# Optimization experiments

Measured on AMD Instinct MI355X. Metric: run time of the kernel, lower is better.

## Reference

```python
import jax, jax.numpy as jnp
import numpy as np

OUT, IN = 11008, 4096
B, S = 8, 32


def setup_inputs() -> dict:
    key = jax.random.key(0)
    k_x, k_w, k_s, k_b = jax.random.split(key, 4)
    x = jax.random.normal(k_x, (B, S, IN), dtype=jnp.float32).astype(jnp.float16)
    # int8 weight storage (symmetric quant range [-128, 127])
    w_int8 = jax.random.randint(k_w, (OUT, IN), -128, 128, dtype=jnp.int32).astype(jnp.int8)
    # per-output-channel scale, small positive values typical of int8 quant
    scale = jax.random.uniform(k_s, (OUT,), dtype=jnp.float32) * 0.01 + 1e-4
    bias = (jax.random.normal(k_b, (OUT,), dtype=jnp.float32) * 0.02).astype(jnp.float16)
    return {"x": x, "w_int8": w_int8, "scale": scale, "bias": bias}


def reference(x, w_int8, scale, bias):
    # w_fp[o, i] = int8_weight[o, i] * scale[o]   (on-the-fly dequant)
    w = w_int8.astype(jnp.float32) * scale[:, None]          # [OUT, IN] fp32
    # F.linear: out = x @ w.T + bias, computed in fp32
    out = jnp.einsum('bsi,oi->bso', x.astype(jnp.float32), w) + bias.astype(jnp.float32)
    return out.astype(x.dtype)                                # cast back to x.dtype (fp16)
```

## Files before the change

kernel.cpp:

```cpp
#include <hip/hip_runtime.h>
#include <hip/hip_bf16.h>
#include <stdint.h>

typedef __attribute__((ext_vector_type(8))) __bf16 bf16x8;
typedef __attribute__((ext_vector_type(4))) float f32x4;

constexpr int K_DIM = 4096;
constexpr int N_DIM = 11008;
constexpr int M_DIM = 256;
constexpr int TN = 32;
constexpr int BK = 64;
constexpr int NT = 256;
constexpr int KT_ALL = K_DIM / BK;
constexpr int KSPLIT = 3;

__device__ __forceinline__ bf16x8 cvt8(const float4 u0, const float4 u1) {
  bf16x8 v;
  v[0] = (__bf16)u0.x; v[1] = (__bf16)u0.y; v[2] = (__bf16)u0.z; v[3] = (__bf16)u0.w;
  v[4] = (__bf16)u1.x; v[5] = (__bf16)u1.y; v[6] = (__bf16)u1.z; v[7] = (__bf16)u1.w;
  return v;
}

__global__ void cvt_x_kernel(const float* __restrict__ x, __bf16* __restrict__ ws) {
  const int t = blockIdx.x * 256 + threadIdx.x;
  const int m = t & 255;
  const int k8 = t >> 8;
  const float* src = x + (size_t)m * K_DIM + k8 * 8;
  const float4 u0 = ((const float4*)src)[0];
  const float4 u1 = ((const float4*)src)[1];
  *(bf16x8*)(ws + (size_t)t * 8) = cvt8(u0, u1);
}

template<bool USE_WS>
__global__ __launch_bounds__(NT, 3) void int8_linear_kernel(
    const float* __restrict__ x,
    const __bf16* __restrict__ xws,
    const int*   __restrict__ w,
    const float* __restrict__ scale,
    const float* __restrict__ bias,
    float*       __restrict__ out)
{
  __shared__ __bf16 Ws[2][TN * BK];

  const int tid  = threadIdx.x;
  const int lane = tid & 63;
  const int wv   = tid >> 6;
  const int quad = lane >> 4;
  const int l16  = lane & 15;
  const int n_base = blockIdx.x * TN;
  const int kc     = blockIdx.y;

  const int t0 = (kc * KT_ALL) / KSPLIT;
  const int t1 = ((kc + 1) * KT_ALL) / KSPLIT;
  const int ntile = t1 - t0;
  const int k0 = t0 * BK;

  const int wrow  = tid >> 3;
  const int wc    = tid & 7;
  const int wslot = wc ^ (wrow & 7);
  const int* wptr = w + (int64_t)(n_base + wrow) * K_DIM + k0 + wc * 8;

  const __bf16* aptr = xws + (size_t)(k0 / 8 + quad) * (M_DIM * 8) + (wv * 64 + l16) * 8;
  const float* fptr = x + (int64_t)(wv * 64 + l16) * K_DIM + k0 + quad * 8;

  f32x4 acc[4][2];
#pragma unroll
  for (int i = 0; i < 4; ++i)
#pragma unroll
    for (int j = 0; j < 2; ++j) acc[i][j] = (f32x4){0.f, 0.f, 0.f, 0.f};

  int wr[8];
  bf16x8 ar0[8], ar1[8];

  auto wload = [&](int t) {
    const int4* p = (const int4*)(wptr + t * BK);
    const int4 u0 = p[0], u1 = p[1];
    wr[0] = u0.x; wr[1] = u0.y; wr[2] = u0.z; wr[3] = u0.w;
    wr[4] = u1.x; wr[5] = u1.y; wr[6] = u1.z; wr[7] = u1.w;
  };
  auto commitW = [&](__bf16* wbuf) {
    bf16x8 v;
#pragma unroll
    for (int j = 0; j < 8; ++j) v[j] = (__bf16)(float)wr[j];
    *(bf16x8*)(wbuf + wrow * BK + wslot * 8) = v;
  };
  auto aload = [&](int t, bf16x8* ar) {
    if (USE_WS) {
#pragma unroll
      for (int ks = 0; ks < 2; ++ks)
#pragma unroll
        for (int mi = 0; mi < 4; ++mi)
          ar[ks * 4 + mi] =
              *(const bf16x8*)(aptr + (size_t)(t * 8 + ks * 4) * (M_DIM * 8) + mi * 128);
    } else {
#pragma unroll
      for (int ks = 0; ks < 2; ++ks)
#pragma unroll
        for (int mi = 0; mi < 4; ++mi) {
          const float* s = fptr + (int64_t)mi * 16 * K_DIM + t * BK + ks * 32;
          ar[ks * 4 + mi] = cvt8(((const float4*)s)[0], ((const float4*)s)[1]);
        }
    }
  };
  auto compute = [&](const bf16x8* ar, const __bf16* wbuf) {
#pragma unroll
    for (int ks = 0; ks < 2; ++ks) {
      bf16x8 b[2];
#pragma unroll
      for (int ni = 0; ni < 2; ++ni) {
        const int n = ni * 16 + l16;
        const int slot = (ks * 4 + quad) ^ (n & 7);
        b[ni] = *(const bf16x8*)(wbuf + n * BK + slot * 8);
      }
#pragma unroll
      for (int mi = 0; mi < 4; ++mi)
#pragma unroll
        for (int ni = 0; ni < 2; ++ni)
          acc[mi][ni] = __builtin_amdgcn_mfma_f32_16x16x32_bf16(
              ar[ks * 4 + mi], b[ni], acc[mi][ni], 0, 0, 0);
    }
  };

  wload(0);
  commitW(Ws[0]);
  aload(0, ar0);

  int t = 0;
  for (; t + 2 <= ntile; t += 2) {
    {
      __syncthreads();
      aload(t + 1, ar1);
      wload(t + 1);
      compute(ar0, Ws[0]);
      commitW(Ws[1]);
    }
    {
      __syncthreads();
      if (t + 2 < ntile) { aload(t + 2, ar0); wload(t + 2); }
      compute(ar1, Ws[1]);
      if (t + 2 < ntile) commitW(Ws[0]);
    }
  }
  if (t < ntile) {
    __syncthreads();
    compute(ar0, Ws[0]);
  }

#pragma unroll
  for (int ni = 0; ni < 2; ++ni) {
    const int col = n_base + ni * 16 + l16;
    const float sc = scale[col];
    const float bi = (kc == 0) ? bias[col] : 0.0f;
#pragma unroll
    for (int mi = 0; mi < 4; ++mi) {
      const int row0 = wv * 64 + mi * 16 + quad * 4;
#pragma unroll
      for (int r = 0; r < 4; ++r)
        unsafeAtomicAdd(out + (int64_t)(row0 + r) * N_DIM + col,
                        acc[mi][ni][r] * sc + bi);
    }
  }
}

extern "C" void kernel_launch(void* const* d_in, const int* in_sizes, int n_in,
                              void* d_out, int out_size, void* d_ws, size_t ws_size,
                              hipStream_t stream) {
  const float* x     = (const float*)d_in[0];
  const int*   w     = (const int*)d_in[1];
  const float* scale = (const float*)d_in[2];
  const float* bias  = (const float*)d_in[3];
  float* out = (float*)d_out;

  __bf16* xws = (__bf16*)d_ws;
  const bool use_ws = ws_size >= (size_t)M_DIM * K_DIM * sizeof(__bf16);

  hipMemsetAsync(out, 0, (size_t)M_DIM * N_DIM * sizeof(float), stream);

  dim3 grid(N_DIM / TN, KSPLIT), block(NT);
  if (use_ws) {
    cvt_x_kernel<<<M_DIM * K_DIM / (256 * 8), 256, 0, stream>>>(x, xws);
    int8_linear_kernel<true><<<grid, block, 0, stream>>>(x, xws, w, scale, bias, out);
  } else {
    int8_linear_kernel<false><<<grid, block, 0, stream>>>(x, xws, w, scale, bias, out);
  }
}
```

Measured before the change: 304.9 us.

## Stage activations in LDS with direct global-to-LDS loads and widen N tile

The N tile grows from 32 to 128 columns and the 256-row activation tile is now staged in shared memory through global_load_lds with an XOR swizzle, instead of each wave loading A fragments into registers. The activation workspace becomes plain row-major, so the conversion kernel simplifies. Split-K rises from 3 to 6 and the occupancy hint drops from 3 to 2. The aim is to reuse each A tile across more columns and cut the redundant global activation traffic. In exchange there are more accumulator registers, two barriers per k-step, and A staging that is no longer double-buffered, so load latency is less hidden.

```diff
diff --git a/kernel.cpp b/kernel.cpp
--- a/kernel.cpp
+++ b/kernel.cpp
@@ -8,11 +8,18 @@
 constexpr int K_DIM = 4096;
 constexpr int N_DIM = 11008;
 constexpr int M_DIM = 256;
-constexpr int TN = 32;
+constexpr int TM = 256;
+constexpr int TN = 128;
 constexpr int BK = 64;
 constexpr int NT = 256;
 constexpr int KT_ALL = K_DIM / BK;
-constexpr int KSPLIT = 3;
+constexpr int KSPLIT = 6;
+
+__device__ __forceinline__ void gload_lds16(const __bf16* gptr, __bf16* lptr) {
+  __builtin_amdgcn_global_load_lds(
+      (const __attribute__((address_space(1))) uint32_t*)gptr,
+      (__attribute__((address_space(3))) uint32_t*)lptr, 16, 0, 0);
+}
 
 __device__ __forceinline__ bf16x8 cvt8(const float4 u0, const float4 u1) {
   bf16x8 v;
@@ -22,17 +29,14 @@
 }
 
 __global__ void cvt_x_kernel(const float* __restrict__ x, __bf16* __restrict__ ws) {
-  const int t = blockIdx.x * 256 + threadIdx.x;
-  const int m = t & 255;
-  const int k8 = t >> 8;
-  const float* src = x + (size_t)m * K_DIM + k8 * 8;
-  const float4 u0 = ((const float4*)src)[0];
-  const float4 u1 = ((const float4*)src)[1];
-  *(bf16x8*)(ws + (size_t)t * 8) = cvt8(u0, u1);
+  const int i = (blockIdx.x * 256 + threadIdx.x) * 8;
+  const float4 u0 = ((const float4*)(x + i))[0];
+  const float4 u1 = ((const float4*)(x + i))[1];
+  *(bf16x8*)(ws + i) = cvt8(u0, u1);
 }
 
 template<bool USE_WS>
-__global__ __launch_bounds__(NT, 3) void int8_linear_kernel(
+__global__ __launch_bounds__(NT, 2) void int8_linear_kernel(
     const float* __restrict__ x,
     const __bf16* __restrict__ xws,
     const int*   __restrict__ w,
@@ -40,13 +44,16 @@
     const float* __restrict__ bias,
     float*       __restrict__ out)
 {
-  __shared__ __bf16 Ws[2][TN * BK];
+  __shared__ __bf16 As[TM * BK];
+  __shared__ __bf16 Wsh[2][TN * BK];
 
   const int tid  = threadIdx.x;
   const int lane = tid & 63;
   const int wv   = tid >> 6;
   const int quad = lane >> 4;
   const int l16  = lane & 15;
+  const int wm   = wv >> 1;
+  const int wn   = wv & 1;
   const int n_base = blockIdx.x * TN;
   const int kc     = blockIdx.y;
 
@@ -55,105 +62,107 @@
   const int ntile = t1 - t0;
   const int k0 = t0 * BK;
 
-  const int wrow  = tid >> 3;
-  const int wc    = tid & 7;
-  const int wslot = wc ^ (wrow & 7);
-  const int* wptr = w + (int64_t)(n_base + wrow) * K_DIM + k0 + wc * 8;
+  const int wrow = tid >> 1;
+  const int wc0  = (tid & 1) * 4;
+  const int* wptr = w + (int64_t)(n_base + wrow) * K_DIM + k0 + wc0 * 8;
 
-  const __bf16* aptr = xws + (size_t)(k0 / 8 + quad) * (M_DIM * 8) + (wv * 64 + l16) * 8;
-  const float* fptr = x + (int64_t)(wv * 64 + l16) * K_DIM + k0 + quad * 8;
+  f32x4 acc[8][4];
+#pragma unroll
+  for (int i = 0; i < 8; ++i)
+#pragma unroll
+    for (int j = 0; j < 4; ++j) acc[i][j] = (f32x4){0.f, 0.f, 0.f, 0.f};
 
-  f32x4 acc[4][2];
-#pragma unroll
-  for (int i = 0; i < 4; ++i)
-#pragma unroll
-    for (int j = 0; j < 2; ++j) acc[i][j] = (f32x4){0.f, 0.f, 0.f, 0.f};
-
-  int wr[8];
-  bf16x8 ar0[8], ar1[8];
-
+  int4 wr[8];
   auto wload = [&](int t) {
     const int4* p = (const int4*)(wptr + t * BK);
-    const int4 u0 = p[0], u1 = p[1];
-    wr[0] = u0.x; wr[1] = u0.y; wr[2] = u0.z; wr[3] = u0.w;
-    wr[4] = u1.x; wr[5] = u1.y; wr[6] = u1.z; wr[7] = u1.w;
+#pragma unroll
+    for (int j = 0; j < 8; ++j) wr[j] = p[j];
   };
   auto commitW = [&](__bf16* wbuf) {
-    bf16x8 v;
 #pragma unroll
-    for (int j = 0; j < 8; ++j) v[j] = (__bf16)(float)wr[j];
-    *(bf16x8*)(wbuf + wrow * BK + wslot * 8) = v;
+    for (int j = 0; j < 4; ++j) {
+      const int4 a = wr[j * 2], b = wr[j * 2 + 1];
+      bf16x8 v;
+      v[0] = (__bf16)(float)a.x; v[1] = (__bf16)(float)a.y;
+      v[2] = (__bf16)(float)a.z; v[3] = (__bf16)(float)a.w;
+      v[4] = (__bf16)(float)b.x; v[5] = (__bf16)(float)b.y;
+      v[6] = (__bf16)(float)b.z; v[7] = (__bf16)(float)b.w;
+      const int slot = (wc0 + j) ^ (wrow & 7);
+      *(bf16x8*)(wbuf + wrow * BK + slot * 8) = v;
+    }
   };
-  auto aload = [&](int t, bf16x8* ar) {
+  auto a_stage = [&](int t) {
     if (USE_WS) {
 #pragma unroll
-      for (int ks = 0; ks < 2; ++ks)
-#pragma unroll
-        for (int mi = 0; mi < 4; ++mi)
-          ar[ks * 4 + mi] =
-              *(const bf16x8*)(aptr + (size_t)(t * 8 + ks * 4) * (M_DIM * 8) + mi * 128);
+      for (int j = 0; j < 8; ++j) {
+        const int c = j * 256 + tid;
+        const int row = c >> 3;
+        const int k8 = (c & 7) ^ (row & 7);
+        gload_lds16(xws + (int64_t)row * K_DIM + (t0 + t) * BK + k8 * 8, As + c * 8);
+      }
     } else {
 #pragma unroll
-      for (int ks = 0; ks < 2; ++ks)
-#pragma unroll
-        for (int mi = 0; mi < 4; ++mi) {
-          const float* s = fptr + (int64_t)mi * 16 * K_DIM + t * BK + ks * 32;
-          ar[ks * 4 + mi] = cvt8(((const float4*)s)[0], ((const float4*)s)[1]);
-        }
+      for (int j = 0; j < 8; ++j) {
+        const int c = j * 256 + tid;
+        const int row = c >> 3;
+        const int k8 = c & 7;
+        const float* s = x + (int64_t)row * K_DIM + (t0 + t) * BK + k8 * 8;
+        const bf16x8 v = cvt8(((const float4*)s)[0], ((const float4*)s)[1]);
+        const int slot = k8 ^ (row & 7);
+        *(bf16x8*)(As + row * BK + slot * 8) = v;
+      }
     }
   };
-  auto compute = [&](const bf16x8* ar, const __bf16* wbuf) {
+  auto compute = [&](const __bf16* wbuf) {
 #pragma unroll
     for (int ks = 0; ks < 2; ++ks) {
-      bf16x8 b[2];
+      bf16x8 a[8], b[4];
 #pragma unroll
-      for (int ni = 0; ni < 2; ++ni) {
-        const int n = ni * 16 + l16;
+      for (int mi = 0; mi < 8; ++mi) {
+        const int m = wm * 128 + mi * 16 + l16;
+        const int slot = (ks * 4 + quad) ^ (m & 7);
+        a[mi] = *(const bf16x8*)(As + m * BK + slot * 8);
+      }
+#pragma unroll
+      for (int ni = 0; ni < 4; ++ni) {
+        const int n = wn * 64 + ni * 16 + l16;
         const int slot = (ks * 4 + quad) ^ (n & 7);
         b[ni] = *(const bf16x8*)(wbuf + n * BK + slot * 8);
       }
 #pragma unroll
-      for (int mi = 0; mi < 4; ++mi)
+      for (int mi = 0; mi < 8; ++mi)
 #pragma unroll
-        for (int ni = 0; ni < 2; ++ni)
+        for (int ni = 0; ni < 4; ++ni)
           acc[mi][ni] = __builtin_amdgcn_mfma_f32_16x16x32_bf16(
-              ar[ks * 4 + mi], b[ni], acc[mi][ni], 0, 0, 0);
+              a[mi], b[ni], acc[mi][ni], 0, 0, 0);
     }
   };
 
   wload(0);
-  commitW(Ws[0]);
-  aload(0, ar0);
+  commitW(Wsh[0]);
+  a_stage(0);
+  __syncthreads();
 
-  int t = 0;
-  for (; t + 2 <= ntile; t += 2) {
-    {
+  for (int t = 0; t < ntile; ++t) {
+    const bool more = (t + 1 < ntile);
+    if (more) wload(t + 1);
+    compute(Wsh[t & 1]);
+    if (more) {
+      commitW(Wsh[(t + 1) & 1]);
       __syncthreads();
-      aload(t + 1, ar1);
-      wload(t + 1);
-      compute(ar0, Ws[0]);
-      commitW(Ws[1]);
+      a_stage(t + 1);
+      __syncthreads();
     }
-    {
-      __syncthreads();
-      if (t + 2 < ntile) { aload(t + 2, ar0); wload(t + 2); }
-      compute(ar1, Ws[1]);
-      if (t + 2 < ntile) commitW(Ws[0]);
-    }
-  }
-  if (t < ntile) {
-    __syncthreads();
-    compute(ar0, Ws[0]);
   }
 
 #pragma unroll
-  for (int ni = 0; ni < 2; ++ni) {
-    const int col = n_base + ni * 16 + l16;
+  for (int ni = 0; ni < 4; ++ni) {
+    const int col = n_base + wn * 64 + ni * 16 + l16;
     const float sc = scale[col];
     const float bi = (kc == 0) ? bias[col] : 0.0f;
 #pragma unroll
-    for (int mi = 0; mi < 4; ++mi) {
-      const int row0 = wv * 64 + mi * 16 + quad * 4;
+    for (int mi = 0; mi < 8; ++mi) {
+      const int row0 = wm * 128 + mi * 16 + quad * 4;
 #pragma unroll
       for (int r = 0; r < 4; ++r)
         unsafeAtomicAdd(out + (int64_t)(row0 + r) * N_DIM + col,
```

After: 326.8 us. +7.2%, slower.
